# Kernel optimization log

Hardware: AMD Instinct MI355X
Metric: run time of the kernel (lower is better)

Reference implementation:

```python
import jax, jax.numpy as jnp
import numpy as np

K = 16

def _local_cov(points):
    # points: [B, N, 3]. FoldingNet-style local covariance feature.
    xx = jnp.sum(points * points, axis=-1)                       # [B,N]
    inner = jnp.einsum('bnd,bmd->bnm', points, points)           # [B,N,N]
    pd = -xx[:, :, None] + 2.0 * inner - xx[:, None, :]          # negative sq dist
    _, idx = jax.lax.top_k(pd, K)                                # [B,N,K] nearest first (self at 0)
    n0 = jnp.take_along_axis(points, idx[:, :, 0][:, :, None], axis=1)  # [B,N,3]
    n1 = jnp.take_along_axis(points, idx[:, :, 1][:, :, None], axis=1)  # [B,N,3]
    cov = n0[..., :, None] * n1[..., None, :]                    # [B,N,3,3] outer product
    B, N = points.shape[0], points.shape[1]
    return jnp.concatenate([points, cov.reshape(B, N, 9)], axis=-1)     # [B,N,12]

def _stage(x, w1, b1, wr, br, w2, b2):
    h = jax.nn.relu(x @ w1 + b1)
    h = jax.nn.relu(h + (h @ wr + br))   # ResidualLinearLayer then ReLU
    return h @ w2 + b2                   # [B,N,1]

def setup_inputs() -> dict:
    key = jax.random.key(0)
    ks = jax.random.split(key, 16)
    B, N, F = 8, 4096, 512
    s = 0.02
    d = {
        'latent': jax.random.normal(ks[0], (B, N, F), jnp.float32),
        'reconstructed_points': jax.random.normal(ks[1], (B, 3, N), jnp.float32),
        's1_w1': jax.random.normal(ks[2], (F + 12, F), jnp.float32) * s,
        's1_b1': jnp.zeros((F,), jnp.float32),
        's1_wr': jax.random.normal(ks[3], (F, F), jnp.float32) * s,
        's1_br': jnp.zeros((F,), jnp.float32),
        's1_w2': jax.random.normal(ks[4], (F, 1), jnp.float32) * s,
        's1_b2': jnp.zeros((1,), jnp.float32),
        's2_w1': jax.random.normal(ks[5], (F + 1, F), jnp.float32) * s,
        's2_b1': jnp.zeros((F,), jnp.float32),
        's2_wr': jax.random.normal(ks[6], (F, F), jnp.float32) * s,
        's2_br': jnp.zeros((F,), jnp.float32),
        's2_w2': jax.random.normal(ks[7], (F, 1), jnp.float32) * s,
        's2_b2': jnp.zeros((1,), jnp.float32),
        's3_w1': jax.random.normal(ks[8], (F + 1, F), jnp.float32) * s,
        's3_b1': jnp.zeros((F,), jnp.float32),
        's3_wr': jax.random.normal(ks[9], (F, F), jnp.float32) * s,
        's3_br': jnp.zeros((F,), jnp.float32),
        's3_w2': jax.random.normal(ks[10], (F, 1), jnp.float32) * s,
        's3_b2': jnp.zeros((1,), jnp.float32),
    }
    return d

def reference(latent, reconstructed_points,
              s1_w1, s1_b1, s1_wr, s1_br, s1_w2, s1_b2,
              s2_w1, s2_b1, s2_wr, s2_br, s2_w2, s2_b2,
              s3_w1, s3_b1, s3_wr, s3_br, s3_w2, s3_b2):
    pts = jnp.transpose(reconstructed_points, (0, 2, 1))   # [B,N,3]
    local = _local_cov(pts)                                 # [B,N,12]
    f1 = jnp.concatenate([latent, local], axis=-1)
    std1 = _stage(f1, s1_w1, s1_b1, s1_wr, s1_br, s1_w2, s1_b2)
    f2 = jnp.concatenate([latent, std1], axis=-1)
    std2 = std1 + _stage(f2, s2_w1, s2_b1, s2_wr, s2_br, s2_w2, s2_b2)
    f3 = jnp.concatenate([latent, std2], axis=-1)
    std3 = std2 + _stage(f3, s3_w1, s3_b1, s3_wr, s3_br, s3_w2, s3_b2)
    return std3   # [B,N,1]
```

## Files before the change

kernel.cpp:

```cpp
#include <hip/hip_runtime.h>

typedef __bf16 bf16x8 __attribute__((ext_vector_type(8)));
typedef float f32x16 __attribute__((ext_vector_type(16)));

__device__ __forceinline__ unsigned short f2bf(float f) {
  unsigned u = __float_as_uint(f);
  u += 0x7FFFu + ((u >> 16) & 1u);
  return (unsigned short)(u >> 16);
}

__device__ __forceinline__ void gload_lds16(const void* g, void* l) {
  __builtin_amdgcn_global_load_lds((const __attribute__((address_space(1))) void*)g,
                                   (__attribute__((address_space(3))) void*)l,
                                   16, 0, 0);
}

#define NPTS 4096
#define LDX 576

__global__ __launch_bounds__(256) void convw6_kernel(
    const float* w0, const float* w1, const float* w2,
    const float* r0, const float* r1, const float* r2,
    unsigned short* d0, unsigned short* d1, unsigned short* d2,
    unsigned short* e0, unsigned short* e1, unsigned short* e2) {
  int z = blockIdx.z;
  const float* src; unsigned short* dst; int Ksrc, Kpad, addI;
  switch (z) {
    case 0: src = w0; dst = d0; Ksrc = 524; Kpad = 576; addI = 0; break;
    case 1: src = w1; dst = d1; Ksrc = 513; Kpad = 576; addI = 0; break;
    case 2: src = w2; dst = d2; Ksrc = 513; Kpad = 576; addI = 0; break;
    case 3: src = r0; dst = e0; Ksrc = 512; Kpad = 512; addI = 1; break;
    case 4: src = r1; dst = e1; Ksrc = 512; Kpad = 512; addI = 1; break;
    default: src = r2; dst = e2; Ksrc = 512; Kpad = 512; addI = 1; break;
  }
  int k0 = blockIdx.x * 32;
  if (k0 >= Kpad) return;
  __shared__ float tile[32][33];
  int n0 = blockIdx.y * 32;
  int tx = threadIdx.x & 31, ty = threadIdx.x >> 5;
#pragma unroll
  for (int r = 0; r < 32; r += 8) {
    int k = k0 + ty + r, n = n0 + tx;
    tile[ty + r][tx] = (k < Ksrc) ? src[(size_t)k * 512 + n] : 0.f;
  }
  __syncthreads();
#pragma unroll
  for (int r = 0; r < 32; r += 8) {
    int n = n0 + ty + r, k = k0 + tx;
    float v = tile[tx][ty + r];
    if (addI && n == k) v += 1.0f;
    dst[(size_t)n * Kpad + k] = f2bf(v);
  }
}

__global__ __launch_bounds__(256) void conv_latent_kernel(const float* __restrict__ latent,
                                                          unsigned short* __restrict__ X) {
  size_t idx = (size_t)blockIdx.x * 256 + threadIdx.x;
  size_t m = idx >> 7;
  int c4 = (int)(idx & 127) * 4;
  float4 v = *(const float4*)(latent + m * 512 + c4);
  ushort4 o;
  o.x = f2bf(v.x); o.y = f2bf(v.y); o.z = f2bf(v.z); o.w = f2bf(v.w);
  *(ushort4*)(X + m * LDX + c4) = o;
}

__device__ __forceinline__ void merge1(float& v, int& j, int mk) {
  float ov = __shfl_xor(v, mk); int oj = __shfl_xor(j, mk);
  bool take = (ov > v) || (ov == v && oj < j);
  v = take ? ov : v; j = take ? oj : j;
}

__global__ __launch_bounds__(512) void knn_kernel(const float* __restrict__ rp,
                                                  unsigned short* __restrict__ X) {
  __shared__ float4 P[NPTS];
  int b = blockIdx.y;
  const float* base = rp + (size_t)b * 3 * NPTS;
  for (int j = threadIdx.x; j < NPTS; j += 512) {
    float x = base[j], y = base[NPTS + j], z = base[2 * NPTS + j];
    float xx = __fadd_rn(__fadd_rn(__fmul_rn(x, x), __fmul_rn(y, y)), __fmul_rn(z, z));
    P[j] = make_float4(x, y, z, -xx);
  }
  __syncthreads();
  int wave = threadIdx.x >> 6, lane = threadIdx.x & 63;
  int grp = lane >> 4, slice = lane & 15;
  int il0 = wave * 8 + grp * 2;
  int ia = blockIdx.x * 64 + il0;
  int ib = ia + 1;
  float4 pa = P[ia], pb = P[ib];
  float ax = 2.f * pa.x, ay = 2.f * pa.y, az = 2.f * pa.z;
  float bx = 2.f * pb.x, by = 2.f * pb.y, bz = 2.f * pb.z;
  float va = -3.4e38f, vb = -3.4e38f;
  int ta = 0, tb = 0;
  int sta = ((ia & 15) == slice) ? (ia >> 4) : -1;
  int stb = ((ib & 15) == slice) ? (ib >> 4) : -1;
  const float4* pp = P + slice;
#pragma unroll 8
  for (int t = 0; t < NPTS / 16; ++t) {
    float4 pj = pp[t * 16];
    float ea = __builtin_fmaf(ax, pj.x, __builtin_fmaf(ay, pj.y,
               __builtin_fmaf(az, pj.z, pj.w)));
    float eb = __builtin_fmaf(bx, pj.x, __builtin_fmaf(by, pj.y,
               __builtin_fmaf(bz, pj.z, pj.w)));
    ea = (t == sta) ? -3.4e38f : ea;
    eb = (t == stb) ? -3.4e38f : eb;
    bool ca = ea > va; va = ca ? ea : va; ta = ca ? t : ta;
    bool cb = eb > vb; vb = cb ? eb : vb; tb = cb ? t : tb;
  }
  int ja = ta * 16 + slice, jb = tb * 16 + slice;
#pragma unroll
  for (int mk = 1; mk <= 8; mk <<= 1) {
    merge1(va, ja, mk);
    merge1(vb, jb, mk);
  }
  if (slice == 0) {
#pragma unroll
    for (int p = 0; p < 2; ++p) {
      float4 pi = (p == 0) ? pa : pb;
      float4 p1 = P[(p == 0) ? ja : jb];
      size_t row = (size_t)b * NPTS + ia + p;
      unsigned short* xp = X + row * LDX + 512;
      float vals[12] = { pi.x, pi.y, pi.z,
                         pi.x * p1.x, pi.x * p1.y, pi.x * p1.z,
                         pi.y * p1.x, pi.y * p1.y, pi.y * p1.z,
                         pi.z * p1.x, pi.z * p1.y, pi.z * p1.z };
#pragma unroll
      for (int k = 0; k < 12; ++k) xp[k] = f2bf(vals[k]);
#pragma unroll
      for (int k = 12; k < 32; ++k) xp[k] = 0;
    }
  }
}

#define BM 128
#define BN 128
#define BK 64
#define GRP 520

__global__ __launch_bounds__(256) void gemm_relu_kernel(
    const unsigned short* __restrict__ Xb, const unsigned short* __restrict__ Wt,
    const float* __restrict__ bias, unsigned short* __restrict__ H,
    int K, int ldx, int ldw) {
  __shared__ unsigned short As[16 * GRP];
  __shared__ unsigned short Bs[16 * GRP];
  const int t = threadIdx.x;
  const int wave = t >> 6, lane = t & 63;
  const int m0 = blockIdx.y * BM, n0 = blockIdx.x * BN;
  const int wm = (wave >> 1) * 64, wn = (wave & 1) * 64;
  const int srow = lane >> 3;
  const int sslot = (lane & 7) ^ srow;
  const int l31 = lane & 31, hi = lane >> 5;
  const int w7 = l31 & 7, g2 = l31 >> 3;
  f32x16 acc[2][2] = {};
  for (int kt = 0; kt < K; kt += BK) {
#pragma unroll
    for (int r = 0; r < 4; ++r) {
      int c = r * 4 + wave;
      gload_lds16(Xb + (size_t)(m0 + c * 8 + srow) * ldx + kt + sslot * 8, As + c * GRP);
      gload_lds16(Wt + (size_t)(n0 + c * 8 + srow) * ldw + kt + sslot * 8, Bs + c * GRP);
    }
    __syncthreads();
#pragma unroll
    for (int ks = 0; ks < 4; ++ks) {
      int qx = (ks * 2 + hi) ^ w7;
      bf16x8 a[2], bb[2];
#pragma unroll
      for (int i = 0; i < 2; ++i)
        a[i] = *(const bf16x8*)(As + ((wm >> 3) + i * 4 + g2) * GRP + w7 * 64 + qx * 8);
#pragma unroll
      for (int j = 0; j < 2; ++j)
        bb[j] = *(const bf16x8*)(Bs + ((wn >> 3) + j * 4 + g2) * GRP + w7 * 64 + qx * 8);
#pragma unroll
      for (int i = 0; i < 2; ++i)
#pragma unroll
        for (int j = 0; j < 2; ++j)
          acc[i][j] = __builtin_amdgcn_mfma_f32_32x32x16_bf16(a[i], bb[j], acc[i][j], 0, 0, 0);
    }
    __syncthreads();
  }
#pragma unroll
  for (int j = 0; j < 2; ++j) {
    int col = n0 + wn + j * 32 + l31;
    float bv = bias[col];
#pragma unroll
    for (int i = 0; i < 2; ++i) {
#pragma unroll
      for (int rg = 0; rg < 16; ++rg) {
        int row = m0 + wm + i * 32 + (rg & 3) + 8 * (rg >> 2) + 4 * hi;
        float v = acc[i][j][rg] + bv;
        v = v > 0.f ? v : 0.f;
        H[(size_t)row * 512 + col] = f2bf(v);
      }
    }
  }
}

__global__ __launch_bounds__(256) void gemm_res_kernel(
    const unsigned short* __restrict__ H1, const unsigned short* __restrict__ Wt,
    const float* __restrict__ br, const float* __restrict__ w2,
    float* __restrict__ so) {
  __shared__ unsigned short As[16 * GRP];
  __shared__ unsigned short Bs[16 * GRP];
  const int t = threadIdx.x;
  const int wave = t >> 6, lane = t & 63;
  const int m0 = blockIdx.y * BM, n0 = blockIdx.x * BN;
  const int wm = (wave >> 1) * 64, wn = (wave & 1) * 64;
  const int srow = lane >> 3;
  const int sslot = (lane & 7) ^ srow;
  const int l31 = lane & 31, hi = lane >> 5;
  const int w7 = l31 & 7, g2 = l31 >> 3;
  f32x16 acc[2][2] = {};
  for (int kt = 0; kt < 512; kt += BK) {
#pragma unroll
    for (int r = 0; r < 4; ++r) {
      int c = r * 4 + wave;
      gload_lds16(H1 + (size_t)(m0 + c * 8 + srow) * 512 + kt + sslot * 8, As + c * GRP);
      gload_lds16(Wt + (size_t)(n0 + c * 8 + srow) * 512 + kt + sslot * 8, Bs + c * GRP);
    }
    __syncthreads();
#pragma unroll
    for (int ks = 0; ks < 4; ++ks) {
      int qx = (ks * 2 + hi) ^ w7;
      bf16x8 a[2], bb[2];
#pragma unroll
      for (int i = 0; i < 2; ++i)
        a[i] = *(const bf16x8*)(As + ((wm >> 3) + i * 4 + g2) * GRP + w7 * 64 + qx * 8);
#pragma unroll
      for (int j = 0; j < 2; ++j)
        bb[j] = *(const bf16x8*)(Bs + ((wn >> 3) + j * 4 + g2) * GRP + w7 * 64 + qx * 8);
#pragma unroll
      for (int i = 0; i < 2; ++i)
#pragma unroll
        for (int j = 0; j < 2; ++j)
          acc[i][j] = __builtin_amdgcn_mfma_f32_32x32x16_bf16(a[i], bb[j], acc[i][j], 0, 0, 0);
    }
    __syncthreads();
  }
  float pr[2][16];
#pragma unroll
  for (int i = 0; i < 2; ++i)
#pragma unroll
    for (int rg = 0; rg < 16; ++rg) pr[i][rg] = 0.f;
#pragma unroll
  for (int j = 0; j < 2; ++j) {
    int col = n0 + wn + j * 32 + l31;
    float bv = br[col], wv = w2[col];
#pragma unroll
    for (int i = 0; i < 2; ++i)
#pragma unroll
      for (int rg = 0; rg < 16; ++rg) {
        float v = acc[i][j][rg] + bv;
        v = v > 0.f ? v : 0.f;
        pr[i][rg] += v * wv;
      }
  }
#pragma unroll
  for (int i = 0; i < 2; ++i)
#pragma unroll
    for (int rg = 0; rg < 16; ++rg) {
      float s = pr[i][rg];
      s += __shfl_xor(s, 1); s += __shfl_xor(s, 2); s += __shfl_xor(s, 4);
      s += __shfl_xor(s, 8); s += __shfl_xor(s, 16);
      if (l31 == 0) {
        int row = m0 + wm + i * 32 + (rg & 3) + 8 * (rg >> 2) + 4 * hi;
        atomicAdd(&so[row], s);
      }
    }
}

__global__ __launch_bounds__(256) void init_so_kernel(float* so, const float* b2) {
  int m = blockIdx.x * 256 + threadIdx.x;
  so[m] = b2[0];
}
__global__ __launch_bounds__(256) void update_kernel(float* std_cum, float* so,
                                                     unsigned short* X,
                                                     const float* b2_next, int first) {
  int m = blockIdx.x * 256 + threadIdx.x;
  float s = so[m];
  if (!first) s += std_cum[m];
  std_cum[m] = s;
  unsigned short* xp = X + (size_t)m * LDX + 512;
  xp[0] = f2bf(s);
#pragma unroll
  for (int k = 1; k < 12; ++k) xp[k] = 0;
  so[m] = b2_next[0];
}
__global__ __launch_bounds__(256) void finalize_kernel(float* out, const float* std_cum,
                                                       const float* so) {
  int m = blockIdx.x * 256 + threadIdx.x;
  out[m] = std_cum[m] + so[m];
}

extern "C" void kernel_launch(void* const* d_in, const int* in_sizes, int n_in,
                              void* d_out, int out_size, void* d_ws, size_t ws_size,
                              hipStream_t stream) {
  const int B = 8, N = NPTS, M = B * N;
  const float* latent = (const float*)d_in[0];
  const float* rp = (const float*)d_in[1];
  const float* w1[3] = {(const float*)d_in[2], (const float*)d_in[8], (const float*)d_in[14]};
  const float* b1[3] = {(const float*)d_in[3], (const float*)d_in[9], (const float*)d_in[15]};
  const float* wr[3] = {(const float*)d_in[4], (const float*)d_in[10], (const float*)d_in[16]};
  const float* br[3] = {(const float*)d_in[5], (const float*)d_in[11], (const float*)d_in[17]};
  const float* w2[3] = {(const float*)d_in[6], (const float*)d_in[12], (const float*)d_in[18]};
  const float* b2[3] = {(const float*)d_in[7], (const float*)d_in[13], (const float*)d_in[19]};

  char* ws = (char*)d_ws;
  auto carve = [&](size_t bytes) {
    char* p = ws;
    ws += (bytes + 255) & ~(size_t)255;
    return p;
  };
  unsigned short* X  = (unsigned short*)carve((size_t)M * LDX * 2);
  unsigned short* H1 = (unsigned short*)carve((size_t)M * 512 * 2);
  unsigned short* W1t[3], *Wrt[3];
  for (int s = 0; s < 3; ++s) W1t[s] = (unsigned short*)carve((size_t)512 * LDX * 2);
  for (int s = 0; s < 3; ++s) Wrt[s] = (unsigned short*)carve((size_t)512 * 512 * 2);
  float* std_cum = (float*)carve((size_t)M * 4);
  float* so      = (float*)carve((size_t)M * 4);

  convw6_kernel<<<dim3(LDX / 32, 16, 6), 256, 0, stream>>>(
      w1[0], w1[1], w1[2], wr[0], wr[1], wr[2],
      W1t[0], W1t[1], W1t[2], Wrt[0], Wrt[1], Wrt[2]);
  conv_latent_kernel<<<(M * 128) / 256, 256, 0, stream>>>(latent, X);
  knn_kernel<<<dim3(N / 64, B), 512, 0, stream>>>(rp, X);
  init_so_kernel<<<M / 256, 256, 0, stream>>>(so, b2[0]);

  for (int s = 0; s < 3; ++s) {
    gemm_relu_kernel<<<dim3(4, M / BM), 256, 0, stream>>>(X, W1t[s], b1[s], H1, LDX, LDX, LDX);
    gemm_res_kernel<<<dim3(4, M / BM), 256, 0, stream>>>(H1, Wrt[s], br[s], w2[s], so);
    if (s < 2)
      update_kernel<<<M / 256, 256, 0, stream>>>(std_cum, so, X, b2[s + 1], s == 0 ? 1 : 0);
  }
  finalize_kernel<<<M / 256, 256, 0, stream>>>((float*)d_out, std_cum, so);
}
```

Before: 394.0 us.

## Fuse both per-stage GEMMs into one kernel keeping hidden activations in LDS

Replaces the separate ReLU GEMM and residual GEMM kernels with a single fused_stage_kernel. Each 64-row block computes the first-layer hidden tile chunk by chunk into LDS and immediately accumulates it into the residual GEMM, finishing with the w2 dot product reduced in shared memory. This removes the H1 round trip through global memory, the global atomics and the init_so launch, with b2 now added inside the kernel. In exchange the tiles are smaller (64x64 per block step, one MFMA per wave per k-slice), weights are re-streamed by every 64-row block, barriers are more frequent and register pressure rises from the 8-tile accumulator.

```diff
diff --git a/kernel.cpp b/kernel.cpp
--- a/kernel.cpp
+++ b/kernel.cpp
@@ -131,149 +131,129 @@
   }
 }
 
-#define BM 128
-#define BN 128
-#define BK 64
-#define GRP 520
-
-__global__ __launch_bounds__(256) void gemm_relu_kernel(
-    const unsigned short* __restrict__ Xb, const unsigned short* __restrict__ Wt,
-    const float* __restrict__ bias, unsigned short* __restrict__ H,
-    int K, int ldx, int ldw) {
-  __shared__ unsigned short As[16 * GRP];
-  __shared__ unsigned short Bs[16 * GRP];
+__global__ __launch_bounds__(256, 2) void fused_stage_kernel(
+    const unsigned short* __restrict__ Xb, const unsigned short* __restrict__ W1t,
+    const float* __restrict__ b1, const unsigned short* __restrict__ Wrt,
+    const float* __restrict__ br, const float* __restrict__ w2,
+    const float* __restrict__ b2, float* __restrict__ so) {
+  __shared__ unsigned short As[8 * 512];
+  __shared__ unsigned short Bs[8 * 512];
+  __shared__ unsigned short H1c[8 * 512];
+  __shared__ unsigned short B2s[8 * 512];
+  __shared__ float sored[64];
   const int t = threadIdx.x;
   const int wave = t >> 6, lane = t & 63;
-  const int m0 = blockIdx.y * BM, n0 = blockIdx.x * BN;
-  const int wm = (wave >> 1) * 64, wn = (wave & 1) * 64;
+  const int m0 = blockIdx.x * 64;
+  const int r0 = (wave & 1) * 32;
+  const int c0 = (wave >> 1) * 32;
   const int srow = lane >> 3;
   const int sslot = (lane & 7) ^ srow;
   const int l31 = lane & 31, hi = lane >> 5;
   const int w7 = l31 & 7, g2 = l31 >> 3;
-  f32x16 acc[2][2] = {};
-  for (int kt = 0; kt < K; kt += BK) {
-#pragma unroll
-    for (int r = 0; r < 4; ++r) {
-      int c = r * 4 + wave;
-      gload_lds16(Xb + (size_t)(m0 + c * 8 + srow) * ldx + kt + sslot * 8, As + c * GRP);
-      gload_lds16(Wt + (size_t)(n0 + c * 8 + srow) * ldw + kt + sslot * 8, Bs + c * GRP);
+  const int ag = (r0 >> 3) + g2;
+  if (t < 64) sored[t] = 0.f;
+
+  float brv[8], w2v[8];
+#pragma unroll
+  for (int j = 0; j < 8; ++j) {
+    brv[j] = br[j * 64 + c0 + l31];
+    w2v[j] = w2[j * 64 + c0 + l31];
+  }
+
+  f32x16 acc2[8];
+#pragma unroll
+  for (int j = 0; j < 8; ++j)
+#pragma unroll
+    for (int r = 0; r < 16; ++r) acc2[j][r] = 0.f;
+
+  for (int nt = 0; nt < 8; ++nt) {
+    f32x16 acc1;
+#pragma unroll
+    for (int r = 0; r < 16; ++r) acc1[r] = 0.f;
+    float b1v = b1[nt * 64 + c0 + l31];
+    for (int kt = 0; kt < 9; ++kt) {
+#pragma unroll
+      for (int r = 0; r < 2; ++r) {
+        int c = r * 4 + wave;
+        gload_lds16(Xb + (size_t)(m0 + c * 8 + srow) * LDX + kt * 64 + sslot * 8,
+                    As + c * 512);
+        gload_lds16(W1t + (size_t)(nt * 64 + c * 8 + srow) * LDX + kt * 64 + sslot * 8,
+                    Bs + c * 512);
+      }
+      __syncthreads();
+#pragma unroll
+      for (int ks = 0; ks < 4; ++ks) {
+        int slot = (ks * 2 + hi) ^ w7;
+        bf16x8 a = *(const bf16x8*)(As + ag * 512 + w7 * 64 + slot * 8);
+        bf16x8 b = *(const bf16x8*)(Bs + ((c0 >> 3) + g2) * 512 + w7 * 64 + slot * 8);
+        acc1 = __builtin_amdgcn_mfma_f32_32x32x16_bf16(a, b, acc1, 0, 0, 0);
+      }
+      __syncthreads();
+    }
+    {
+      int col = c0 + l31;
+      int cch = col >> 3, cel = col & 7;
+#pragma unroll
+      for (int rg = 0; rg < 16; ++rg) {
+        int m = r0 + (rg & 3) + 8 * (rg >> 2) + 4 * hi;
+        float v = acc1[rg] + b1v;
+        v = v > 0.f ? v : 0.f;
+        H1c[(m >> 3) * 512 + (m & 7) * 64 + (cch ^ (m & 7)) * 8 + cel] = f2bf(v);
+      }
     }
     __syncthreads();
+    bf16x8 a2[4];
 #pragma unroll
     for (int ks = 0; ks < 4; ++ks) {
-      int qx = (ks * 2 + hi) ^ w7;
-      bf16x8 a[2], bb[2];
-#pragma unroll
-      for (int i = 0; i < 2; ++i)
-        a[i] = *(const bf16x8*)(As + ((wm >> 3) + i * 4 + g2) * GRP + w7 * 64 + qx * 8);
-#pragma unroll
-      for (int j = 0; j < 2; ++j)
-        bb[j] = *(const bf16x8*)(Bs + ((wn >> 3) + j * 4 + g2) * GRP + w7 * 64 + qx * 8);
-#pragma unroll
-      for (int i = 0; i < 2; ++i)
-#pragma unroll
-        for (int j = 0; j < 2; ++j)
-          acc[i][j] = __builtin_amdgcn_mfma_f32_32x32x16_bf16(a[i], bb[j], acc[i][j], 0, 0, 0);
-    }
-    __syncthreads();
-  }
-#pragma unroll
-  for (int j = 0; j < 2; ++j) {
-    int col = n0 + wn + j * 32 + l31;
-    float bv = bias[col];
-#pragma unroll
-    for (int i = 0; i < 2; ++i) {
-#pragma unroll
-      for (int rg = 0; rg < 16; ++rg) {
-        int row = m0 + wm + i * 32 + (rg & 3) + 8 * (rg >> 2) + 4 * hi;
-        float v = acc[i][j][rg] + bv;
-        v = v > 0.f ? v : 0.f;
-        H[(size_t)row * 512 + col] = f2bf(v);
-      }
-    }
-  }
-}
-
-__global__ __launch_bounds__(256) void gemm_res_kernel(
-    const unsigned short* __restrict__ H1, const unsigned short* __restrict__ Wt,
-    const float* __restrict__ br, const float* __restrict__ w2,
-    float* __restrict__ so) {
-  __shared__ unsigned short As[16 * GRP];
-  __shared__ unsigned short Bs[16 * GRP];
-  const int t = threadIdx.x;
-  const int wave = t >> 6, lane = t & 63;
-  const int m0 = blockIdx.y * BM, n0 = blockIdx.x * BN;
-  const int wm = (wave >> 1) * 64, wn = (wave & 1) * 64;
-  const int srow = lane >> 3;
-  const int sslot = (lane & 7) ^ srow;
-  const int l31 = lane & 31, hi = lane >> 5;
-  const int w7 = l31 & 7, g2 = l31 >> 3;
-  f32x16 acc[2][2] = {};
-  for (int kt = 0; kt < 512; kt += BK) {
-#pragma unroll
-    for (int r = 0; r < 4; ++r) {
-      int c = r * 4 + wave;
-      gload_lds16(H1 + (size_t)(m0 + c * 8 + srow) * 512 + kt + sslot * 8, As + c * GRP);
-      gload_lds16(Wt + (size_t)(n0 + c * 8 + srow) * 512 + kt + sslot * 8, Bs + c * GRP);
-    }
-    __syncthreads();
-#pragma unroll
-    for (int ks = 0; ks < 4; ++ks) {
-      int qx = (ks * 2 + hi) ^ w7;
-      bf16x8 a[2], bb[2];
-#pragma unroll
-      for (int i = 0; i < 2; ++i)
-        a[i] = *(const bf16x8*)(As + ((wm >> 3) + i * 4 + g2) * GRP + w7 * 64 + qx * 8);
-#pragma unroll
-      for (int j = 0; j < 2; ++j)
-        bb[j] = *(const bf16x8*)(Bs + ((wn >> 3) + j * 4 + g2) * GRP + w7 * 64 + qx * 8);
-#pragma unroll
-      for (int i = 0; i < 2; ++i)
-#pragma unroll
-        for (int j = 0; j < 2; ++j)
-          acc[i][j] = __builtin_amdgcn_mfma_f32_32x32x16_bf16(a[i], bb[j], acc[i][j], 0, 0, 0);
-    }
-    __syncthreads();
-  }
-  float pr[2][16];
-#pragma unroll
-  for (int i = 0; i < 2; ++i)
-#pragma unroll
-    for (int rg = 0; rg < 16; ++rg) pr[i][rg] = 0.f;
-#pragma unroll
-  for (int j = 0; j < 2; ++j) {
-    int col = n0 + wn + j * 32 + l31;
-    float bv = br[col], wv = w2[col];
-#pragma unroll
-    for (int i = 0; i < 2; ++i)
-#pragma unroll
-      for (int rg = 0; rg < 16; ++rg) {
-        float v = acc[i][j][rg] + bv;
-        v = v > 0.f ? v : 0.f;
-        pr[i][rg] += v * wv;
-      }
-  }
-#pragma unroll
-  for (int i = 0; i < 2; ++i)
+      int slot = (ks * 2 + hi) ^ w7;
+      a2[ks] = *(const bf16x8*)(H1c + ag * 512 + w7 * 64 + slot * 8);
+    }
+#pragma unroll
+    for (int jnt = 0; jnt < 8; ++jnt) {
+#pragma unroll
+      for (int r = 0; r < 2; ++r) {
+        int c = r * 4 + wave;
+        gload_lds16(Wrt + (size_t)(jnt * 64 + c * 8 + srow) * 512 + nt * 64 + sslot * 8,
+                    B2s + c * 512);
+      }
+      __syncthreads();
+#pragma unroll
+      for (int ks = 0; ks < 4; ++ks) {
+        int slot = (ks * 2 + hi) ^ w7;
+        bf16x8 b = *(const bf16x8*)(B2s + ((c0 >> 3) + g2) * 512 + w7 * 64 + slot * 8);
+        acc2[jnt] = __builtin_amdgcn_mfma_f32_32x32x16_bf16(a2[ks], b, acc2[jnt], 0, 0, 0);
+      }
+      __syncthreads();
+    }
+  }
+  float partial[16];
+#pragma unroll
+  for (int rg = 0; rg < 16; ++rg) partial[rg] = 0.f;
+#pragma unroll
+  for (int jnt = 0; jnt < 8; ++jnt)
 #pragma unroll
     for (int rg = 0; rg < 16; ++rg) {
-      float s = pr[i][rg];
-      s += __shfl_xor(s, 1); s += __shfl_xor(s, 2); s += __shfl_xor(s, 4);
-      s += __shfl_xor(s, 8); s += __shfl_xor(s, 16);
-      if (l31 == 0) {
-        int row = m0 + wm + i * 32 + (rg & 3) + 8 * (rg >> 2) + 4 * hi;
-        atomicAdd(&so[row], s);
-      }
-    }
-}
-
-__global__ __launch_bounds__(256) void init_so_kernel(float* so, const float* b2) {
-  int m = blockIdx.x * 256 + threadIdx.x;
-  so[m] = b2[0];
-}
-__global__ __launch_bounds__(256) void update_kernel(float* std_cum, float* so,
-                                                     unsigned short* X,
-                                                     const float* b2_next, int first) {
+      float v = acc2[jnt][rg] + brv[jnt];
+      v = v > 0.f ? v : 0.f;
+      partial[rg] = __builtin_fmaf(v, w2v[jnt], partial[rg]);
+    }
+#pragma unroll
+  for (int rg = 0; rg < 16; ++rg) {
+    float s = partial[rg];
+    s += __shfl_xor(s, 1); s += __shfl_xor(s, 2); s += __shfl_xor(s, 4);
+    s += __shfl_xor(s, 8); s += __shfl_xor(s, 16);
+    if (l31 == 0) {
+      int m = r0 + (rg & 3) + 8 * (rg >> 2) + 4 * hi;
+      atomicAdd(&sored[m], s);
+    }
+  }
+  __syncthreads();
+  float b2v = b2[0];
+  if (t < 64) so[m0 + t] = sored[t] + b2v;
+}
+
+__global__ __launch_bounds__(256) void update_kernel(float* std_cum, const float* so,
+                                                     unsigned short* X, int first) {
   int m = blockIdx.x * 256 + threadIdx.x;
   float s = so[m];
   if (!first) s += std_cum[m];
@@ -282,7 +262,6 @@
   xp[0] = f2bf(s);
 #pragma unroll
   for (int k = 1; k < 12; ++k) xp[k] = 0;
-  so[m] = b2_next[0];
 }
 __global__ __launch_bounds__(256) void finalize_kernel(float* out, const float* std_cum,
                                                        const float* so) {
@@ -309,8 +288,7 @@
     ws += (bytes + 255) & ~(size_t)255;
     return p;
   };
-  unsigned short* X  = (unsigned short*)carve((size_t)M * LDX * 2);
-  unsigned short* H1 = (unsigned short*)carve((size_t)M * 512 * 2);
+  unsigned short* X = (unsigned short*)carve((size_t)M * LDX * 2);
   unsigned short* W1t[3], *Wrt[3];
   for (int s = 0; s < 3; ++s) W1t[s] = (unsigned short*)carve((size_t)512 * LDX * 2);
   for (int s = 0; s < 3; ++s) Wrt[s] = (unsigned short*)carve((size_t)512 * 512 * 2);
@@ -322,13 +300,12 @@
       W1t[0], W1t[1], W1t[2], Wrt[0], Wrt[1], Wrt[2]);
   conv_latent_kernel<<<(M * 128) / 256, 256, 0, stream>>>(latent, X);
   knn_kernel<<<dim3(N / 64, B), 512, 0, stream>>>(rp, X);
-  init_so_kernel<<<M / 256, 256, 0, stream>>>(so, b2[0]);
 
   for (int s = 0; s < 3; ++s) {
-    gemm_relu_kernel<<<dim3(4, M / BM), 256, 0, stream>>>(X, W1t[s], b1[s], H1, LDX, LDX, LDX);
-    gemm_res_kernel<<<dim3(4, M / BM), 256, 0, stream>>>(H1, Wrt[s], br[s], w2[s], so);
+    fused_stage_kernel<<<M / 64, 256, 0, stream>>>(X, W1t[s], b1[s], Wrt[s], br[s],
+                                                   w2[s], b2[s], so);
     if (s < 2)
-      update_kernel<<<M / 256, 256, 0, stream>>>(std_cum, so, X, b2[s + 1], s == 0 ? 1 : 0);
+      update_kernel<<<M / 256, 256, 0, stream>>>(std_cum, so, X, s == 0 ? 1 : 0);
   }
   finalize_kernel<<<M / 256, 256, 0, stream>>>((float*)d_out, std_cum, so);
 }
```

New measurement: 536.2 us. 36.1% more time.

## Replace direct global-to-LDS loads with register-prefetched padded LDS tiles

Applied to the files above, without the earlier changes.

Both GEMM kernels drop the async global_load_lds path with an XOR-swizzled layout. They now load the next K tile into registers while MFMAs run on the current tile, then store it to a padded row-major LDS tile (stride 72) that avoids bank conflicts. The intent is to hide global load latency behind compute. In exchange it uses more VGPRs, adds an extra barrier per iteration, and routes data through registers, which can cost occupancy.

```diff
diff --git a/kernel.cpp b/kernel.cpp
--- a/kernel.cpp
+++ b/kernel.cpp
@@ -7,12 +7,6 @@
   unsigned u = __float_as_uint(f);
   u += 0x7FFFu + ((u >> 16) & 1u);
   return (unsigned short)(u >> 16);
-}
-
-__device__ __forceinline__ void gload_lds16(const void* g, void* l) {
-  __builtin_amdgcn_global_load_lds((const __attribute__((address_space(1))) void*)g,
-                                   (__attribute__((address_space(3))) void*)l,
-                                   16, 0, 0);
 }
 
 #define NPTS 4096
@@ -134,41 +128,54 @@
 #define BM 128
 #define BN 128
 #define BK 64
-#define GRP 520
+#define LDT 72
 
 __global__ __launch_bounds__(256) void gemm_relu_kernel(
     const unsigned short* __restrict__ Xb, const unsigned short* __restrict__ Wt,
     const float* __restrict__ bias, unsigned short* __restrict__ H,
     int K, int ldx, int ldw) {
-  __shared__ unsigned short As[16 * GRP];
-  __shared__ unsigned short Bs[16 * GRP];
+  __shared__ unsigned short As[BM * LDT];
+  __shared__ unsigned short Bs[BN * LDT];
   const int t = threadIdx.x;
   const int wave = t >> 6, lane = t & 63;
   const int m0 = blockIdx.y * BM, n0 = blockIdx.x * BN;
   const int wm = (wave >> 1) * 64, wn = (wave & 1) * 64;
-  const int srow = lane >> 3;
-  const int sslot = (lane & 7) ^ srow;
   const int l31 = lane & 31, hi = lane >> 5;
-  const int w7 = l31 & 7, g2 = l31 >> 3;
+  int srow[4], sc[4];
+#pragma unroll
+  for (int r = 0; r < 4; ++r) { int id = t + r * 256; srow[r] = id >> 3; sc[r] = (id & 7) * 8; }
   f32x16 acc[2][2] = {};
-  for (int kt = 0; kt < K; kt += BK) {
-#pragma unroll
-    for (int r = 0; r < 4; ++r) {
-      int c = r * 4 + wave;
-      gload_lds16(Xb + (size_t)(m0 + c * 8 + srow) * ldx + kt + sslot * 8, As + c * GRP);
-      gload_lds16(Wt + (size_t)(n0 + c * 8 + srow) * ldw + kt + sslot * 8, Bs + c * GRP);
-    }
-    __syncthreads();
+  int4 pa[4], pb[4];
+#pragma unroll
+  for (int r = 0; r < 4; ++r) {
+    pa[r] = *(const int4*)(Xb + (size_t)(m0 + srow[r]) * ldx + sc[r]);
+    pb[r] = *(const int4*)(Wt + (size_t)(n0 + srow[r]) * ldw + sc[r]);
+  }
+#pragma unroll
+  for (int r = 0; r < 4; ++r) {
+    *(int4*)(As + srow[r] * LDT + sc[r]) = pa[r];
+    *(int4*)(Bs + srow[r] * LDT + sc[r]) = pb[r];
+  }
+  __syncthreads();
+  const int NK = K / BK;
+  for (int kt = 0; kt < NK; ++kt) {
+    if (kt + 1 < NK) {
+      int ko = (kt + 1) * BK;
+#pragma unroll
+      for (int r = 0; r < 4; ++r) {
+        pa[r] = *(const int4*)(Xb + (size_t)(m0 + srow[r]) * ldx + ko + sc[r]);
+        pb[r] = *(const int4*)(Wt + (size_t)(n0 + srow[r]) * ldw + ko + sc[r]);
+      }
+    }
 #pragma unroll
     for (int ks = 0; ks < 4; ++ks) {
-      int qx = (ks * 2 + hi) ^ w7;
       bf16x8 a[2], bb[2];
 #pragma unroll
       for (int i = 0; i < 2; ++i)
-        a[i] = *(const bf16x8*)(As + ((wm >> 3) + i * 4 + g2) * GRP + w7 * 64 + qx * 8);
+        a[i] = *(const bf16x8*)(As + (wm + i * 32 + l31) * LDT + ks * 16 + hi * 8);
 #pragma unroll
       for (int j = 0; j < 2; ++j)
-        bb[j] = *(const bf16x8*)(Bs + ((wn >> 3) + j * 4 + g2) * GRP + w7 * 64 + qx * 8);
+        bb[j] = *(const bf16x8*)(Bs + (wn + j * 32 + l31) * LDT + ks * 16 + hi * 8);
 #pragma unroll
       for (int i = 0; i < 2; ++i)
 #pragma unroll
@@ -176,6 +183,14 @@
           acc[i][j] = __builtin_amdgcn_mfma_f32_32x32x16_bf16(a[i], bb[j], acc[i][j], 0, 0, 0);
     }
     __syncthreads();
+    if (kt + 1 < NK) {
+#pragma unroll
+      for (int r = 0; r < 4; ++r) {
+        *(int4*)(As + srow[r] * LDT + sc[r]) = pa[r];
+        *(int4*)(Bs + srow[r] * LDT + sc[r]) = pb[r];
+      }
+      __syncthreads();
+    }
   }
 #pragma unroll
   for (int j = 0; j < 2; ++j) {
@@ -198,35 +213,47 @@
     const unsigned short* __restrict__ H1, const unsigned short* __restrict__ Wt,
     const float* __restrict__ br, const float* __restrict__ w2,
     float* __restrict__ so) {
-  __shared__ unsigned short As[16 * GRP];
-  __shared__ unsigned short Bs[16 * GRP];
+  __shared__ unsigned short As[BM * LDT];
+  __shared__ unsigned short Bs[BN * LDT];
   const int t = threadIdx.x;
   const int wave = t >> 6, lane = t & 63;
   const int m0 = blockIdx.y * BM, n0 = blockIdx.x * BN;
   const int wm = (wave >> 1) * 64, wn = (wave & 1) * 64;
-  const int srow = lane >> 3;
-  const int sslot = (lane & 7) ^ srow;
   const int l31 = lane & 31, hi = lane >> 5;
-  const int w7 = l31 & 7, g2 = l31 >> 3;
+  int srow[4], sc[4];
+#pragma unroll
+  for (int r = 0; r < 4; ++r) { int id = t + r * 256; srow[r] = id >> 3; sc[r] = (id & 7) * 8; }
   f32x16 acc[2][2] = {};
-  for (int kt = 0; kt < 512; kt += BK) {
-#pragma unroll
-    for (int r = 0; r < 4; ++r) {
-      int c = r * 4 + wave;
-      gload_lds16(H1 + (size_t)(m0 + c * 8 + srow) * 512 + kt + sslot * 8, As + c * GRP);
-      gload_lds16(Wt + (size_t)(n0 + c * 8 + srow) * 512 + kt + sslot * 8, Bs + c * GRP);
-    }
-    __syncthreads();
+  int4 pa[4], pb[4];
+#pragma unroll
+  for (int r = 0; r < 4; ++r) {
+    pa[r] = *(const int4*)(H1 + (size_t)(m0 + srow[r]) * 512 + sc[r]);
+    pb[r] = *(const int4*)(Wt + (size_t)(n0 + srow[r]) * 512 + sc[r]);
+  }
+#pragma unroll
+  for (int r = 0; r < 4; ++r) {
+    *(int4*)(As + srow[r] * LDT + sc[r]) = pa[r];
+    *(int4*)(Bs + srow[r] * LDT + sc[r]) = pb[r];
+  }
+  __syncthreads();
+  for (int kt = 0; kt < 8; ++kt) {
+    if (kt + 1 < 8) {
+      int ko = (kt + 1) * BK;
+#pragma unroll
+      for (int r = 0; r < 4; ++r) {
+        pa[r] = *(const int4*)(H1 + (size_t)(m0 + srow[r]) * 512 + ko + sc[r]);
+        pb[r] = *(const int4*)(Wt + (size_t)(n0 + srow[r]) * 512 + ko + sc[r]);
+      }
+    }
 #pragma unroll
     for (int ks = 0; ks < 4; ++ks) {
-      int qx = (ks * 2 + hi) ^ w7;
       bf16x8 a[2], bb[2];
 #pragma unroll
       for (int i = 0; i < 2; ++i)
-        a[i] = *(const bf16x8*)(As + ((wm >> 3) + i * 4 + g2) * GRP + w7 * 64 + qx * 8);
+        a[i] = *(const bf16x8*)(As + (wm + i * 32 + l31) * LDT + ks * 16 + hi * 8);
 #pragma unroll
       for (int j = 0; j < 2; ++j)
-        bb[j] = *(const bf16x8*)(Bs + ((wn >> 3) + j * 4 + g2) * GRP + w7 * 64 + qx * 8);
+        bb[j] = *(const bf16x8*)(Bs + (wn + j * 32 + l31) * LDT + ks * 16 + hi * 8);
 #pragma unroll
       for (int i = 0; i < 2; ++i)
 #pragma unroll
@@ -234,6 +261,14 @@
           acc[i][j] = __builtin_amdgcn_mfma_f32_32x32x16_bf16(a[i], bb[j], acc[i][j], 0, 0, 0);
     }
     __syncthreads();
+    if (kt + 1 < 8) {
+#pragma unroll
+      for (int r = 0; r < 4; ++r) {
+        *(int4*)(As + srow[r] * LDT + sc[r]) = pa[r];
+        *(int4*)(Bs + srow[r] * LDT + sc[r]) = pb[r];
+      }
+      __syncthreads();
+    }
   }
   float pr[2][16];
 #pragma unroll
```

Result: slower. 707.5 us (+79.6%).
